# Kernel tuning notes

Measured on AMD Instinct MI355X. Metric: run time of the kernel, lower is better.

## Reference

```python
import jax, jax.numpy as jnp
import numpy as np

B = 32        # decode batch (one new token per sequence)
S = 4096      # kv cache length per sequence
H = 32        # query heads
G = 2         # kv groups (multi-query groups)
D = 128       # head dim (kv_channels)
ROT = D // 2  # rotary dim = 64, is_neox_style=False (GPT-J interleaved)
HID = 4096    # hidden size
QKV = (H + 2 * G) * D  # 4608
BASE = 10000.0


def setup_inputs() -> dict:
    key = jax.random.key(0)
    ks = jax.random.split(key, 7)
    return {
        "hidden_states": jax.random.normal(ks[0], (B, HID), jnp.float32),
        "positions": jax.random.randint(ks[1], (B,), 0, S, jnp.int32),
        "k_cache": jax.random.normal(ks[2], (B, S, G, D), jnp.float32) * 0.5,
        "v_cache": jax.random.normal(ks[3], (B, S, G, D), jnp.float32) * 0.5,
        "W_qkv": jax.random.normal(ks[4], (HID, QKV), jnp.float32) * 0.02,
        "b_qkv": jax.random.normal(ks[5], (QKV,), jnp.float32) * 0.02,
        "W_dense": jax.random.normal(ks[6], (H * D, HID), jnp.float32) * 0.02,
    }


def _apply_rope(x, pos):
    # x: [b, n_heads, D]; GPT-J style interleaved rotation on first ROT dims
    inv_freq = 1.0 / (BASE ** (jnp.arange(0, ROT, 2, dtype=jnp.float32) / ROT))  # [ROT//2]
    freqs = pos[:, None].astype(jnp.float32) * inv_freq                          # [b, ROT//2]
    cos = jnp.cos(freqs)[:, None, :]
    sin = jnp.sin(freqs)[:, None, :]
    xr, xp = x[..., :ROT], x[..., ROT:]
    x1, x2 = xr[..., 0::2], xr[..., 1::2]
    o1 = x1 * cos - x2 * sin
    o2 = x2 * cos + x1 * sin
    rot = jnp.stack([o1, o2], axis=-1).reshape(x.shape[:-1] + (ROT,))
    return jnp.concatenate([rot, xp], axis=-1)


def reference(hidden_states, positions, k_cache, v_cache, W_qkv, b_qkv, W_dense):
    # fused QKV projection (MQA split: H query heads, G kv groups)
    qkv = hidden_states @ W_qkv + b_qkv                     # [B, QKV]
    q = qkv[:, : H * D].reshape(B, H, D)
    k = qkv[:, H * D : (H + G) * D].reshape(B, G, D)
    v = qkv[:, (H + G) * D :].reshape(B, G, D)

    # inline RoPE on q and new k
    q = _apply_rope(q, positions)
    k = _apply_rope(k, positions)

    # write new k/v into cache at the current position (paged-cache write)
    b_idx = jnp.arange(B)
    kc = k_cache.at[b_idx, positions].set(k)                # [B, S, G, D]
    vc = v_cache.at[b_idx, positions].set(v)

    # grouped-query attention over the cache, causal via context length
    scale = jnp.float32(D) ** -0.5
    qg = q.reshape(B, G, H // G, D)                         # map head h -> group h // (H/G)
    logits = jnp.einsum("bghd,bsgd->bghs", qg, kc) * scale  # [B, G, H/G, S]
    valid = jnp.arange(S)[None, :] <= positions[:, None]    # [B, S]
    logits = jnp.where(valid[:, None, None, :], logits, jnp.float32(-1e9))
    probs = jax.nn.softmax(logits, axis=-1)
    ctx = jnp.einsum("bghs,bsgd->bghd", probs, vc).reshape(B, H * D)

    return ctx @ W_dense                                    # [B, HID]
```

## Files before the change

kernel.cpp:

```cpp
#include <hip/hip_runtime.h>
#include <math.h>

#define Bz 32
#define Sz 4096
#define Hz 32
#define Gz 2
#define Dz 128
#define HIDz 4096
#define QKVz 4608
#define NCHc 16

static __device__ __forceinline__ void fma4(float4& a, float s, const float4& v) {
  a.x = fmaf(s, v.x, a.x);
  a.y = fmaf(s, v.y, a.y);
  a.z = fmaf(s, v.z, a.z);
  a.w = fmaf(s, v.w, a.w);
}
static __device__ __forceinline__ float dot4(const float4& a, const float4& b, float acc) {
  return fmaf(a.x, b.x, fmaf(a.y, b.y, fmaf(a.z, b.z, fmaf(a.w, b.w, acc))));
}
static __device__ __forceinline__ void gload16(const float* src, float* ldst) {
  __builtin_amdgcn_global_load_lds(
      (const __attribute__((address_space(1))) void*)src,
      (__attribute__((address_space(3))) void*)ldst, 16, 0, 0);
}

__global__ __launch_bounds__(256) void gemm_partial(
    const float* __restrict__ X, const float* __restrict__ W,
    float* __restrict__ part, int K, int N, int KH) {
  extern __shared__ float hl[];
  const int stride = KH + 4;
  const int t = threadIdx.x;
  const int k0 = blockIdx.y * KH;
  const int cols4 = KH >> 2;
  const int total4 = Bz * cols4;
  for (int fi = t; fi < total4; fi += 256) {
    const int row = fi / cols4;
    const int c4 = fi - row * cols4;
    const float4 v = *(const float4*)&X[(size_t)row * K + k0 + c4 * 4];
    *(float4*)&hl[row * stride + c4 * 4] = v;
  }
  __syncthreads();
  const int jl = t & 31;
  const int b0 = (t >> 5) * 4;
  const int j = blockIdx.x * 128 + jl * 4;
  float4 acc[4];
  #pragma unroll
  for (int i = 0; i < 4; i++) acc[i] = make_float4(0.f, 0.f, 0.f, 0.f);
  #pragma unroll 4
  for (int kk = 0; kk < KH; kk += 4) {
    const float4 w0 = *(const float4*)&W[(size_t)(k0 + kk + 0) * N + j];
    const float4 w1 = *(const float4*)&W[(size_t)(k0 + kk + 1) * N + j];
    const float4 w2 = *(const float4*)&W[(size_t)(k0 + kk + 2) * N + j];
    const float4 w3 = *(const float4*)&W[(size_t)(k0 + kk + 3) * N + j];
    #pragma unroll
    for (int bi = 0; bi < 4; bi++) {
      const float4 hb = *(const float4*)&hl[(b0 + bi) * stride + kk];
      fma4(acc[bi], hb.x, w0);
      fma4(acc[bi], hb.y, w1);
      fma4(acc[bi], hb.z, w2);
      fma4(acc[bi], hb.w, w3);
    }
  }
  #pragma unroll
  for (int bi = 0; bi < 4; bi++) {
    *(float4*)&part[((size_t)blockIdx.y * Bz + b0 + bi) * N + j] = acc[bi];
  }
}

__global__ __launch_bounds__(256) void qkv_finish(
    const float* __restrict__ part, const float* __restrict__ bias,
    const int* __restrict__ positions, int KT,
    float* __restrict__ qrot, float* __restrict__ krot, float* __restrict__ vnew) {
  const int t = threadIdx.x;
  const int b = blockIdx.x;
  const int head = blockIdx.y * 4 + (t >> 6);
  const int tp = t & 63;
  const int j0 = head * Dz + tp * 2;
  float s0 = bias[j0];
  float s1 = bias[j0 + 1];
  for (int kt = 0; kt < KT; kt++) {
    const float2 p = *(const float2*)&part[((size_t)kt * Bz + b) * QKVz + j0];
    s0 += p.x;
    s1 += p.y;
  }
  float o0 = s0, o1 = s1;
  if (head < Hz + Gz && tp < 32) {
    const float invf = exp2f(-(float)tp * (13.287712379549449f / 32.0f));
    const float a = (float)positions[b] * invf;
    float sn, cs;
    sincosf(a, &sn, &cs);
    o0 = s0 * cs - s1 * sn;
    o1 = s1 * cs + s0 * sn;
  }
  if (head < Hz) {
    const float sc = 0.08838834764831845f;
    float2 o = make_float2(o0 * sc, o1 * sc);
    *(float2*)&qrot[((size_t)b * Hz + head) * Dz + tp * 2] = o;
  } else if (head < Hz + Gz) {
    float2 o = make_float2(o0, o1);
    *(float2*)&krot[((size_t)b * Gz + (head - Hz)) * Dz + tp * 2] = o;
  } else {
    float2 o = make_float2(s0, s1);
    *(float2*)&vnew[((size_t)b * Gz + (head - Hz - Gz)) * Dz + tp * 2] = o;
  }
}

__global__ __launch_bounds__(256, 2) void attn_unit(
    const float* __restrict__ qrot, const float* __restrict__ kcache,
    const float* __restrict__ vcache, const float* __restrict__ krot,
    const float* __restrict__ vnew, const int* __restrict__ positions,
    float* __restrict__ mbuf, float* __restrict__ lbuf, float* __restrict__ pacc) {
  __shared__ float kb[2][4096];
  __shared__ float vb[2][4096];
  __shared__ float qt[2176];
  __shared__ float pl[4][160];
  __shared__ float ml[128];
  const int g = blockIdx.y, b = blockIdx.z, bx = blockIdx.x;
  const int pos = positions[b];
  const int lt = pos + 1;
  const int blo = (bx * lt) >> 4;
  const int bhi = ((bx + 1) * lt) >> 4;
  const int nr = bhi - blo;
  const int ntile = (nr + 31) >> 5;
  const int t = threadIdx.x;
  const int w = t >> 6, lane = t & 63;
  const int s8 = lane >> 3, c8 = lane & 7;

  for (int i = t; i < 512; i += 256) {
    const int c = i >> 4, h = i & 15;
    const float4 q = *(const float4*)&qrot[((size_t)b * Hz + g * 16 + h) * Dz + c * 4];
    *(float4*)&qt[c * 68 + h * 4] = q;
  }

  const float* krow_new = &krot[((size_t)b * Gz + g) * Dz];
  const float* vrow_new = &vnew[((size_t)b * Gz + g) * Dz];
  const size_t kvb = ((size_t)b * Sz) * (Gz * Dz) + (size_t)g * Dz;

#define STAGE(tile, buf)                                                          \
  { _Pragma("unroll") for (int r4 = 0; r4 < 4; ++r4) {                            \
      const int sg = blo + (tile) * 32 + r4 * 8 + (t >> 5);                       \
      const bool fresh = (sg >= bhi) || (sg == pos);                              \
      const float* kp = fresh ? krow_new : &kcache[kvb + (size_t)sg * (Gz * Dz)]; \
      const float* vp = fresh ? vrow_new : &vcache[kvb + (size_t)sg * (Gz * Dz)]; \
      gload16(kp + (t & 31) * 4, &kb[buf][r4 * 1024 + t * 4]);                    \
      gload16(vp + (t & 31) * 4, &vb[buf][r4 * 1024 + t * 4]); } }

  float m_run[16], l_run[16];
  float2 A2[16];
  #pragma unroll
  for (int h = 0; h < 16; ++h) {
    m_run[h] = -1e30f;
    l_run[h] = 0.f;
    A2[h] = make_float2(0.f, 0.f);
  }

  int cur = 0;
  if (ntile > 0) STAGE(0, 0);
  __syncthreads();

  for (int tile = 0; tile < ntile; ++tile) {
    if (tile + 1 < ntile) STAGE(tile + 1, cur ^ 1);
    const int rbase = tile * 32 + w * 8;
    const bool valid = (rbase + s8) < nr;

    float lp[16];
    #pragma unroll
    for (int h = 0; h < 16; ++h) lp[h] = 0.f;
    float4 kf[4];
    #pragma unroll
    for (int it = 0; it < 4; ++it)
      kf[it] = *(const float4*)&kb[cur][(w * 8 + s8) * 128 + (c8 + it * 8) * 4];
    #pragma unroll
    for (int it = 0; it < 4; ++it) {
      #pragma unroll
      for (int h = 0; h < 16; ++h) {
        const float4 qv = *(const float4*)&qt[(c8 + it * 8) * 68 + h * 4];
        lp[h] = dot4(qv, kf[it], lp[h]);
      }
    }
    #pragma unroll
    for (int h = 0; h < 16; ++h) {
      lp[h] += __shfl_xor(lp[h], 1);
      lp[h] += __shfl_xor(lp[h], 2);
      lp[h] += __shfl_xor(lp[h], 4);
    }
    #pragma unroll
    for (int h = 0; h < 16; ++h) {
      const float lg = valid ? lp[h] : -1e30f;
      float v = lg;
      v = fmaxf(v, __shfl_xor(v, 8));
      v = fmaxf(v, __shfl_xor(v, 16));
      v = fmaxf(v, __shfl_xor(v, 32));
      const float mn = fmaxf(m_run[h], v);
      const float sc = __expf(m_run[h] - mn);
      m_run[h] = mn;
      const float p = valid ? __expf(lg - mn) : 0.f;
      float ts = p;
      ts += __shfl_xor(ts, 8);
      ts += __shfl_xor(ts, 16);
      ts += __shfl_xor(ts, 32);
      l_run[h] = l_run[h] * sc + ts;
      A2[h].x *= sc;
      A2[h].y *= sc;
      lp[h] = p;
    }
    if (c8 == 0) {
      float* pr = &pl[w][s8 * 20];
      *(float4*)&pr[0] = make_float4(lp[0], lp[1], lp[2], lp[3]);
      *(float4*)&pr[4] = make_float4(lp[4], lp[5], lp[6], lp[7]);
      *(float4*)&pr[8] = make_float4(lp[8], lp[9], lp[10], lp[11]);
      *(float4*)&pr[12] = make_float4(lp[12], lp[13], lp[14], lp[15]);
    }
    #pragma unroll
    for (int s = 0; s < 8; ++s) {
      const float2 v2 = *(const float2*)&vb[cur][(w * 8 + s) * 128 + lane * 2];
      const float4 p0 = *(const float4*)&pl[w][s * 20 + 0];
      const float4 p1 = *(const float4*)&pl[w][s * 20 + 4];
      const float4 p2 = *(const float4*)&pl[w][s * 20 + 8];
      const float4 p3 = *(const float4*)&pl[w][s * 20 + 12];
      A2[0].x = fmaf(p0.x, v2.x, A2[0].x);  A2[0].y = fmaf(p0.x, v2.y, A2[0].y);
      A2[1].x = fmaf(p0.y, v2.x, A2[1].x);  A2[1].y = fmaf(p0.y, v2.y, A2[1].y);
      A2[2].x = fmaf(p0.z, v2.x, A2[2].x);  A2[2].y = fmaf(p0.z, v2.y, A2[2].y);
      A2[3].x = fmaf(p0.w, v2.x, A2[3].x);  A2[3].y = fmaf(p0.w, v2.y, A2[3].y);
      A2[4].x = fmaf(p1.x, v2.x, A2[4].x);  A2[4].y = fmaf(p1.x, v2.y, A2[4].y);
      A2[5].x = fmaf(p1.y, v2.x, A2[5].x);  A2[5].y = fmaf(p1.y, v2.y, A2[5].y);
      A2[6].x = fmaf(p1.z, v2.x, A2[6].x);  A2[6].y = fmaf(p1.z, v2.y, A2[6].y);
      A2[7].x = fmaf(p1.w, v2.x, A2[7].x);  A2[7].y = fmaf(p1.w, v2.y, A2[7].y);
      A2[8].x = fmaf(p2.x, v2.x, A2[8].x);  A2[8].y = fmaf(p2.x, v2.y, A2[8].y);
      A2[9].x = fmaf(p2.y, v2.x, A2[9].x);  A2[9].y = fmaf(p2.y, v2.y, A2[9].y);
      A2[10].x = fmaf(p2.z, v2.x, A2[10].x); A2[10].y = fmaf(p2.z, v2.y, A2[10].y);
      A2[11].x = fmaf(p2.w, v2.x, A2[11].x); A2[11].y = fmaf(p2.w, v2.y, A2[11].y);
      A2[12].x = fmaf(p3.x, v2.x, A2[12].x); A2[12].y = fmaf(p3.x, v2.y, A2[12].y);
      A2[13].x = fmaf(p3.y, v2.x, A2[13].x); A2[13].y = fmaf(p3.y, v2.y, A2[13].y);
      A2[14].x = fmaf(p3.z, v2.x, A2[14].x); A2[14].y = fmaf(p3.z, v2.y, A2[14].y);
      A2[15].x = fmaf(p3.w, v2.x, A2[15].x); A2[15].y = fmaf(p3.w, v2.y, A2[15].y);
    }
    __syncthreads();
    cur ^= 1;
  }

  if (lane == 0) {
    #pragma unroll
    for (int h = 0; h < 16; h += 4) {
      *(float4*)&ml[w * 32 + h] = make_float4(m_run[h], m_run[h + 1], m_run[h + 2], m_run[h + 3]);
      *(float4*)&ml[w * 32 + 16 + h] =
          make_float4(l_run[h], l_run[h + 1], l_run[h + 2], l_run[h + 3]);
    }
  }
  __syncthreads();
  float ew[16];
  #pragma unroll
  for (int h = 0; h < 16; ++h) {
    const float ms = fmaxf(fmaxf(ml[h], ml[32 + h]), fmaxf(ml[64 + h], ml[96 + h]));
    ew[h] = __expf(m_run[h] - ms);
  }
  float* Aw = kb[0];
  for (int step = 0; step < 4; ++step) {
    if (w == step) {
      #pragma unroll
      for (int h = 0; h < 16; ++h) {
        float2 x;
        if (step == 0) {
          x = make_float2(ew[h] * A2[h].x, ew[h] * A2[h].y);
        } else {
          x = *(const float2*)&Aw[h * 132 + lane * 2];
          x.x = fmaf(ew[h], A2[h].x, x.x);
          x.y = fmaf(ew[h], A2[h].y, x.y);
        }
        *(float2*)&Aw[h * 132 + lane * 2] = x;
      }
    }
    __syncthreads();
  }
  const size_t cb = (size_t)(b * Gz + g) * NCHc + bx;
  for (int o = t; o < 512; o += 256) {
    const int hh = o >> 5, d4c = o & 31;
    *(float4*)&pacc[cb * 2048 + (size_t)hh * Dz + d4c * 4] =
        *(const float4*)&Aw[hh * 132 + d4c * 4];
  }
  if (t < 16) {
    const int hh = t;
    const float m0 = ml[hh], m1 = ml[32 + hh], m2 = ml[64 + hh], m3 = ml[96 + hh];
    const float msf = fmaxf(fmaxf(m0, m1), fmaxf(m2, m3));
    const float l = __expf(m0 - msf) * ml[16 + hh] + __expf(m1 - msf) * ml[48 + hh] +
                    __expf(m2 - msf) * ml[80 + hh] + __expf(m3 - msf) * ml[112 + hh];
    mbuf[cb * 16 + hh] = msf;
    lbuf[cb * 16 + hh] = l;
  }
#undef STAGE
}

__global__ __launch_bounds__(512) void attn_combine(
    const float* __restrict__ mbuf, const float* __restrict__ lbuf,
    const float* __restrict__ pacc, const int* __restrict__ positions,
    float* __restrict__ ctx) {
  const int bg = blockIdx.x;
  const int b = bg >> 1, g = bg & 1;
  const int t = threadIdx.x;
  const int h = t >> 5, dg = t & 31;
  const size_t mlb = (size_t)bg * NCHc * 16 + h;
  float mstar = -1e30f;
  for (int c = 0; c < NCHc; c++) mstar = fmaxf(mstar, mbuf[mlb + c * 16]);
  float lsum = 0.f;
  float4 A = make_float4(0.f, 0.f, 0.f, 0.f);
  for (int c = 0; c < NCHc; c++) {
    const float wv = __expf(mbuf[mlb + c * 16] - mstar);
    lsum += wv * lbuf[mlb + c * 16];
    const float4 p = *(const float4*)&pacc[((size_t)bg * NCHc + c) * 2048 + (size_t)h * Dz + dg * 4];
    fma4(A, wv, p);
  }
  const float inv = 1.0f / lsum;
  float4 o = make_float4(A.x * inv, A.y * inv, A.z * inv, A.w * inv);
  *(float4*)&ctx[(size_t)b * (Hz * Dz) + (g * 16 + h) * Dz + dg * 4] = o;
}

__global__ __launch_bounds__(256) void reduce_out(
    const float* __restrict__ part, float* __restrict__ out, int KT) {
  const int idx = blockIdx.x * 256 + threadIdx.x;
  const int b = idx >> 12;
  const int j = idx & 4095;
  float s = 0.f;
  for (int kt = 0; kt < KT; kt++) s += part[((size_t)kt * Bz + b) * HIDz + j];
  out[idx] = s;
}

extern "C" void kernel_launch(void* const* d_in, const int* in_sizes, int n_in,
                              void* d_out, int out_size, void* d_ws, size_t ws_size,
                              hipStream_t stream) {
  const float* hidden = (const float*)d_in[0];
  const int* positions = (const int*)d_in[1];
  const float* kcache = (const float*)d_in[2];
  const float* vcache = (const float*)d_in[3];
  const float* Wqkv = (const float*)d_in[4];
  const float* bqkv = (const float*)d_in[5];
  const float* Wd = (const float*)d_in[6];
  float* out = (float*)d_out;

  auto need = [](int KT) -> size_t {
    return (size_t)KT * Bz * QKVz
         + (size_t)Bz * Hz * Dz
         + (size_t)Bz * Gz * Dz * 2
         + (size_t)Bz * Gz * NCHc * 16 * 2
         + (size_t)Bz * Gz * NCHc * 2048
         + (size_t)Bz * HIDz;
  };
  int KT = 32;
  if (need(32) * sizeof(float) > ws_size) KT = 16;
  const int KH = HIDz / KT;

  float* w = (float*)d_ws;
  float* p1 = w;    w += (size_t)KT * Bz * QKVz;
  float* qrot = w;  w += (size_t)Bz * Hz * Dz;
  float* krot = w;  w += (size_t)Bz * Gz * Dz;
  float* vnew = w;  w += (size_t)Bz * Gz * Dz;
  float* mbuf = w;  w += (size_t)Bz * Gz * NCHc * 16;
  float* lbuf = w;  w += (size_t)Bz * Gz * NCHc * 16;
  float* pacc = w;  w += (size_t)Bz * Gz * NCHc * 2048;
  float* ctx = w;

  const size_t smem = (size_t)Bz * (KH + 4) * sizeof(float);

  gemm_partial<<<dim3(QKVz / 128, KT), 256, smem, stream>>>(hidden, Wqkv, p1, HIDz, QKVz, KH);
  qkv_finish<<<dim3(Bz, 9), 256, 0, stream>>>(p1, bqkv, positions, KT, qrot, krot, vnew);
  attn_unit<<<dim3(NCHc, Gz, Bz), 256, 0, stream>>>(qrot, kcache, vcache, krot, vnew, positions,
                                                    mbuf, lbuf, pacc);
  attn_combine<<<dim3(Bz * Gz), 512, 0, stream>>>(mbuf, lbuf, pacc, positions, ctx);
  gemm_partial<<<dim3(HIDz / 128, KT), 256, smem, stream>>>(ctx, Wd, p1, Hz * Dz, HIDz, KH);
  reduce_out<<<dim3(Bz * HIDz / 256), 256, 0, stream>>>(p1, out, KT);
}
```

Measured before the change: 169.6 us.

## Restructure attention unit with per-wave K staging, register Q, and direct V loads

Each wave now stages only its own K rows into a private double-buffered LDS slice. V is read straight from global memory instead of being staged in LDS. Q is held in registers instead of a transposed LDS copy, and the lane mapping is reworked so each lane computes a 4x4 head-by-row block of logits. This removes the block-wide __syncthreads per tile, cuts LDS use, and raises launch bounds to 3 blocks per CU for occupancy. The risks are higher register pressure from the q[4][4] float4 array, uncoalesced or latency-exposed V global loads, and possible races on the per-wave LDS buffers without wave-level barriers.

```diff
diff --git a/kernel.cpp b/kernel.cpp
--- a/kernel.cpp
+++ b/kernel.cpp
@@ -106,15 +106,14 @@
   }
 }
 
-__global__ __launch_bounds__(256, 2) void attn_unit(
+__global__ __launch_bounds__(256, 3) void attn_unit(
     const float* __restrict__ qrot, const float* __restrict__ kcache,
     const float* __restrict__ vcache, const float* __restrict__ krot,
     const float* __restrict__ vnew, const int* __restrict__ positions,
     float* __restrict__ mbuf, float* __restrict__ lbuf, float* __restrict__ pacc) {
-  __shared__ float kb[2][4096];
-  __shared__ float vb[2][4096];
-  __shared__ float qt[2176];
-  __shared__ float pl[4][160];
+  __shared__ float kbw[4][2048];
+  __shared__ float plw[4][128];
+  __shared__ float scw[4][16];
   __shared__ float ml[128];
   const int g = blockIdx.y, b = blockIdx.z, bx = blockIdx.x;
   const int pos = positions[b];
@@ -122,113 +121,133 @@
   const int blo = (bx * lt) >> 4;
   const int bhi = ((bx + 1) * lt) >> 4;
   const int nr = bhi - blo;
-  const int ntile = (nr + 31) >> 5;
-  const int t = threadIdx.x;
-  const int w = t >> 6, lane = t & 63;
-  const int s8 = lane >> 3, c8 = lane & 7;
-
-  for (int i = t; i < 512; i += 256) {
-    const int c = i >> 4, h = i & 15;
-    const float4 q = *(const float4*)&qrot[((size_t)b * Hz + g * 16 + h) * Dz + c * 4];
-    *(float4*)&qt[c * 68 + h * 4] = q;
-  }
-
+  const int t = threadIdx.x, w = t >> 6, lane = t & 63;
+  const int hq = lane >> 4, rq = (lane >> 3) & 1, cq = lane & 7;
+  float* kw = kbw[w];
+  float* plv = plw[w];
+
+  float4 q[4][4];
+  #pragma unroll
+  for (int i = 0; i < 4; ++i) {
+    const float* qp = &qrot[((size_t)b * Hz + g * 16 + hq * 4 + i) * Dz + cq * 4];
+    #pragma unroll
+    for (int j = 0; j < 4; ++j) q[i][j] = *(const float4*)&qp[j * 32];
+  }
   const float* krow_new = &krot[((size_t)b * Gz + g) * Dz];
   const float* vrow_new = &vnew[((size_t)b * Gz + g) * Dz];
   const size_t kvb = ((size_t)b * Sz) * (Gz * Dz) + (size_t)g * Dz;
 
-#define STAGE(tile, buf)                                                          \
-  { _Pragma("unroll") for (int r4 = 0; r4 < 4; ++r4) {                            \
-      const int sg = blo + (tile) * 32 + r4 * 8 + (t >> 5);                       \
-      const bool fresh = (sg >= bhi) || (sg == pos);                              \
-      const float* kp = fresh ? krow_new : &kcache[kvb + (size_t)sg * (Gz * Dz)]; \
-      const float* vp = fresh ? vrow_new : &vcache[kvb + (size_t)sg * (Gz * Dz)]; \
-      gload16(kp + (t & 31) * 4, &kb[buf][r4 * 1024 + t * 4]);                    \
-      gload16(vp + (t & 31) * 4, &vb[buf][r4 * 1024 + t * 4]); } }
-
-  float m_run[16], l_run[16];
+#define STAGE(tile, buf) {                                                         \
+    const int sg_ = blo + (tile) * 32 + w * 8 + (lane >> 3);                       \
+    const bool fr_ = (sg_ >= bhi) || (sg_ == pos);                                 \
+    const float* kp_ = fr_ ? krow_new : &kcache[kvb + (size_t)sg_ * (Gz * Dz)];    \
+    gload16(kp_ + (lane & 7) * 4,      &kw[(buf) * 1024 + 0 * 256 + lane * 4]);    \
+    gload16(kp_ + (lane & 7) * 4 + 32, &kw[(buf) * 1024 + 1 * 256 + lane * 4]);    \
+    gload16(kp_ + (lane & 7) * 4 + 64, &kw[(buf) * 1024 + 2 * 256 + lane * 4]);    \
+    gload16(kp_ + (lane & 7) * 4 + 96, &kw[(buf) * 1024 + 3 * 256 + lane * 4]); }
+
+  float m_run[4], l_run[4];
   float2 A2[16];
   #pragma unroll
-  for (int h = 0; h < 16; ++h) {
-    m_run[h] = -1e30f;
-    l_run[h] = 0.f;
-    A2[h] = make_float2(0.f, 0.f);
-  }
-
+  for (int i = 0; i < 4; ++i) { m_run[i] = -1e30f; l_run[i] = 0.f; }
+  #pragma unroll
+  for (int h = 0; h < 16; ++h) A2[h] = make_float2(0.f, 0.f);
+
+  const int ntw = (nr > w * 8) ? ((nr - w * 8 + 31) >> 5) : 0;
   int cur = 0;
-  if (ntile > 0) STAGE(0, 0);
-  __syncthreads();
-
-  for (int tile = 0; tile < ntile; ++tile) {
-    if (tile + 1 < ntile) STAGE(tile + 1, cur ^ 1);
-    const int rbase = tile * 32 + w * 8;
-    const bool valid = (rbase + s8) < nr;
-
-    float lp[16];
-    #pragma unroll
-    for (int h = 0; h < 16; ++h) lp[h] = 0.f;
-    float4 kf[4];
-    #pragma unroll
-    for (int it = 0; it < 4; ++it)
-      kf[it] = *(const float4*)&kb[cur][(w * 8 + s8) * 128 + (c8 + it * 8) * 4];
-    #pragma unroll
-    for (int it = 0; it < 4; ++it) {
-      #pragma unroll
-      for (int h = 0; h < 16; ++h) {
-        const float4 qv = *(const float4*)&qt[(c8 + it * 8) * 68 + h * 4];
-        lp[h] = dot4(qv, kf[it], lp[h]);
+  if (ntw > 0) STAGE(0, 0);
+  for (int tile = 0; tile < ntw; ++tile) {
+    float lp[4][4];
+    #pragma unroll
+    for (int i = 0; i < 4; ++i)
+      #pragma unroll
+      for (int s = 0; s < 4; ++s) lp[i][s] = 0.f;
+    #pragma unroll
+    for (int j = 0; j < 4; ++j) {
+      float4 kf[4];
+      #pragma unroll
+      for (int s = 0; s < 4; ++s)
+        kf[s] = *(const float4*)&kw[cur * 1024 + j * 256 + ((rq * 4 + s) * 8 + cq) * 4];
+      #pragma unroll
+      for (int i = 0; i < 4; ++i)
+        #pragma unroll
+        for (int s = 0; s < 4; ++s) lp[i][s] = dot4(q[i][j], kf[s], lp[i][s]);
+    }
+    if (tile + 1 < ntw) STAGE(tile + 1, cur ^ 1);
+    #pragma unroll
+    for (int i = 0; i < 4; ++i)
+      #pragma unroll
+      for (int s = 0; s < 4; ++s) {
+        lp[i][s] += __shfl_xor(lp[i][s], 1);
+        lp[i][s] += __shfl_xor(lp[i][s], 2);
+        lp[i][s] += __shfl_xor(lp[i][s], 4);
       }
-    }
-    #pragma unroll
-    for (int h = 0; h < 16; ++h) {
-      lp[h] += __shfl_xor(lp[h], 1);
-      lp[h] += __shfl_xor(lp[h], 2);
-      lp[h] += __shfl_xor(lp[h], 4);
-    }
-    #pragma unroll
-    for (int h = 0; h < 16; ++h) {
-      const float lg = valid ? lp[h] : -1e30f;
-      float v = lg;
-      v = fmaxf(v, __shfl_xor(v, 8));
-      v = fmaxf(v, __shfl_xor(v, 16));
-      v = fmaxf(v, __shfl_xor(v, 32));
-      const float mn = fmaxf(m_run[h], v);
-      const float sc = __expf(m_run[h] - mn);
-      m_run[h] = mn;
-      const float p = valid ? __expf(lg - mn) : 0.f;
-      float ts = p;
+    const int rbase = tile * 32 + w * 8 + rq * 4;
+    #pragma unroll
+    for (int s = 0; s < 4; ++s) {
+      if (rbase + s >= nr) {
+        #pragma unroll
+        for (int i = 0; i < 4; ++i) lp[i][s] = -1e30f;
+      }
+    }
+    float sc[4];
+    #pragma unroll
+    for (int i = 0; i < 4; ++i) {
+      float tm = fmaxf(fmaxf(lp[i][0], lp[i][1]), fmaxf(lp[i][2], lp[i][3]));
+      tm = fmaxf(tm, __shfl_xor(tm, 8));
+      const float mn = fmaxf(m_run[i], tm);
+      sc[i] = __expf(m_run[i] - mn);
+      m_run[i] = mn;
+      float ts = 0.f;
+      #pragma unroll
+      for (int s = 0; s < 4; ++s) {
+        lp[i][s] = __expf(lp[i][s] - mn);
+        ts += lp[i][s];
+      }
       ts += __shfl_xor(ts, 8);
-      ts += __shfl_xor(ts, 16);
-      ts += __shfl_xor(ts, 32);
-      l_run[h] = l_run[h] * sc + ts;
-      A2[h].x *= sc;
-      A2[h].y *= sc;
-      lp[h] = p;
-    }
-    if (c8 == 0) {
-      float* pr = &pl[w][s8 * 20];
-      *(float4*)&pr[0] = make_float4(lp[0], lp[1], lp[2], lp[3]);
-      *(float4*)&pr[4] = make_float4(lp[4], lp[5], lp[6], lp[7]);
-      *(float4*)&pr[8] = make_float4(lp[8], lp[9], lp[10], lp[11]);
-      *(float4*)&pr[12] = make_float4(lp[12], lp[13], lp[14], lp[15]);
+      l_run[i] = l_run[i] * sc[i] + ts;
+    }
+    if (cq == 0) {
+      if (rq == 0) *(float4*)&scw[w][hq * 4] = make_float4(sc[0], sc[1], sc[2], sc[3]);
+      #pragma unroll
+      for (int s = 0; s < 4; ++s)
+        *(float4*)&plv[(rq * 4 + s) * 16 + hq * 4] =
+            make_float4(lp[0][s], lp[1][s], lp[2][s], lp[3][s]);
+    }
+    {
+      const float4 s0 = *(const float4*)&scw[w][0];
+      const float4 s1 = *(const float4*)&scw[w][4];
+      const float4 s2 = *(const float4*)&scw[w][8];
+      const float4 s3 = *(const float4*)&scw[w][12];
+      A2[0].x *= s0.x;  A2[0].y *= s0.x;   A2[1].x *= s0.y;  A2[1].y *= s0.y;
+      A2[2].x *= s0.z;  A2[2].y *= s0.z;   A2[3].x *= s0.w;  A2[3].y *= s0.w;
+      A2[4].x *= s1.x;  A2[4].y *= s1.x;   A2[5].x *= s1.y;  A2[5].y *= s1.y;
+      A2[6].x *= s1.z;  A2[6].y *= s1.z;   A2[7].x *= s1.w;  A2[7].y *= s1.w;
+      A2[8].x *= s2.x;  A2[8].y *= s2.x;   A2[9].x *= s2.y;  A2[9].y *= s2.y;
+      A2[10].x *= s2.z; A2[10].y *= s2.z;  A2[11].x *= s2.w; A2[11].y *= s2.w;
+      A2[12].x *= s3.x; A2[12].y *= s3.x;  A2[13].x *= s3.y; A2[13].y *= s3.y;
+      A2[14].x *= s3.z; A2[14].y *= s3.z;  A2[15].x *= s3.w; A2[15].y *= s3.w;
     }
     #pragma unroll
     for (int s = 0; s < 8; ++s) {
-      const float2 v2 = *(const float2*)&vb[cur][(w * 8 + s) * 128 + lane * 2];
-      const float4 p0 = *(const float4*)&pl[w][s * 20 + 0];
-      const float4 p1 = *(const float4*)&pl[w][s * 20 + 4];
-      const float4 p2 = *(const float4*)&pl[w][s * 20 + 8];
-      const float4 p3 = *(const float4*)&pl[w][s * 20 + 12];
-      A2[0].x = fmaf(p0.x, v2.x, A2[0].x);  A2[0].y = fmaf(p0.x, v2.y, A2[0].y);
-      A2[1].x = fmaf(p0.y, v2.x, A2[1].x);  A2[1].y = fmaf(p0.y, v2.y, A2[1].y);
-      A2[2].x = fmaf(p0.z, v2.x, A2[2].x);  A2[2].y = fmaf(p0.z, v2.y, A2[2].y);
-      A2[3].x = fmaf(p0.w, v2.x, A2[3].x);  A2[3].y = fmaf(p0.w, v2.y, A2[3].y);
-      A2[4].x = fmaf(p1.x, v2.x, A2[4].x);  A2[4].y = fmaf(p1.x, v2.y, A2[4].y);
-      A2[5].x = fmaf(p1.y, v2.x, A2[5].x);  A2[5].y = fmaf(p1.y, v2.y, A2[5].y);
-      A2[6].x = fmaf(p1.z, v2.x, A2[6].x);  A2[6].y = fmaf(p1.z, v2.y, A2[6].y);
-      A2[7].x = fmaf(p1.w, v2.x, A2[7].x);  A2[7].y = fmaf(p1.w, v2.y, A2[7].y);
-      A2[8].x = fmaf(p2.x, v2.x, A2[8].x);  A2[8].y = fmaf(p2.x, v2.y, A2[8].y);
-      A2[9].x = fmaf(p2.y, v2.x, A2[9].x);  A2[9].y = fmaf(p2.y, v2.y, A2[9].y);
+      const int sg = blo + tile * 32 + w * 8 + s;
+      const float* vp = (sg >= bhi || sg == pos) ? vrow_new
+                         : &vcache[kvb + (size_t)sg * (Gz * Dz)];
+      const float2 v2 = *(const float2*)&vp[lane * 2];
+      const float4 p0 = *(const float4*)&plv[s * 16 + 0];
+      const float4 p1 = *(const float4*)&plv[s * 16 + 4];
+      const float4 p2 = *(const float4*)&plv[s * 16 + 8];
+      const float4 p3 = *(const float4*)&plv[s * 16 + 12];
+      A2[0].x = fmaf(p0.x, v2.x, A2[0].x);   A2[0].y = fmaf(p0.x, v2.y, A2[0].y);
+      A2[1].x = fmaf(p0.y, v2.x, A2[1].x);   A2[1].y = fmaf(p0.y, v2.y, A2[1].y);
+      A2[2].x = fmaf(p0.z, v2.x, A2[2].x);   A2[2].y = fmaf(p0.z, v2.y, A2[2].y);
+      A2[3].x = fmaf(p0.w, v2.x, A2[3].x);   A2[3].y = fmaf(p0.w, v2.y, A2[3].y);
+      A2[4].x = fmaf(p1.x, v2.x, A2[4].x);   A2[4].y = fmaf(p1.x, v2.y, A2[4].y);
+      A2[5].x = fmaf(p1.y, v2.x, A2[5].x);   A2[5].y = fmaf(p1.y, v2.y, A2[5].y);
+      A2[6].x = fmaf(p1.z, v2.x, A2[6].x);   A2[6].y = fmaf(p1.z, v2.y, A2[6].y);
+      A2[7].x = fmaf(p1.w, v2.x, A2[7].x);   A2[7].y = fmaf(p1.w, v2.y, A2[7].y);
+      A2[8].x = fmaf(p2.x, v2.x, A2[8].x);   A2[8].y = fmaf(p2.x, v2.y, A2[8].y);
+      A2[9].x = fmaf(p2.y, v2.x, A2[9].x);   A2[9].y = fmaf(p2.y, v2.y, A2[9].y);
       A2[10].x = fmaf(p2.z, v2.x, A2[10].x); A2[10].y = fmaf(p2.z, v2.y, A2[10].y);
       A2[11].x = fmaf(p2.w, v2.x, A2[11].x); A2[11].y = fmaf(p2.w, v2.y, A2[11].y);
       A2[12].x = fmaf(p3.x, v2.x, A2[12].x); A2[12].y = fmaf(p3.x, v2.y, A2[12].y);
@@ -236,26 +255,22 @@
       A2[14].x = fmaf(p3.z, v2.x, A2[14].x); A2[14].y = fmaf(p3.z, v2.y, A2[14].y);
       A2[15].x = fmaf(p3.w, v2.x, A2[15].x); A2[15].y = fmaf(p3.w, v2.y, A2[15].y);
     }
-    __syncthreads();
     cur ^= 1;
   }
 
-  if (lane == 0) {
-    #pragma unroll
-    for (int h = 0; h < 16; h += 4) {
-      *(float4*)&ml[w * 32 + h] = make_float4(m_run[h], m_run[h + 1], m_run[h + 2], m_run[h + 3]);
-      *(float4*)&ml[w * 32 + 16 + h] =
-          make_float4(l_run[h], l_run[h + 1], l_run[h + 2], l_run[h + 3]);
-    }
+  __syncthreads();
+  if (cq == 0 && rq == 0) {
+    *(float4*)&ml[w * 32 + hq * 4] = make_float4(m_run[0], m_run[1], m_run[2], m_run[3]);
+    *(float4*)&ml[w * 32 + 16 + hq * 4] = make_float4(l_run[0], l_run[1], l_run[2], l_run[3]);
   }
   __syncthreads();
   float ew[16];
   #pragma unroll
   for (int h = 0; h < 16; ++h) {
     const float ms = fmaxf(fmaxf(ml[h], ml[32 + h]), fmaxf(ml[64 + h], ml[96 + h]));
-    ew[h] = __expf(m_run[h] - ms);
-  }
-  float* Aw = kb[0];
+    ew[h] = __expf(ml[w * 32 + h] - ms);
+  }
+  float* Aw = &kbw[0][0];
   for (int step = 0; step < 4; ++step) {
     if (w == step) {
       #pragma unroll
```

Measured after the change: 217.9 us. +28.5%, slower.
